# Kernel optimization log

Measured on AMD Instinct MI355X. Metric: run time of the kernel, lower is better.

Reference implementation:

```python
import jax, jax.numpy as jnp
import numpy as np

N = 50000      # nodes
E = 1600000    # edges (avg degree 32)
G = 128        # graphs in batch
NE = 5         # spectral supports (edge_attr channels)
NIN = 16       # input node features
H = 64         # nout1 hidden width
NCLS = 6
BN_EPS = 1e-5


def setup_inputs() -> dict:
    key = jax.random.key(0)
    ks = jax.random.split(key, 12)
    s = 0.1  # weight init scale
    x = jax.random.normal(ks[0], (N, NIN), dtype=jnp.float32)
    edge_index = jax.random.randint(ks[1], (2, E), 0, N, dtype=jnp.int32)
    edge_attr = jax.random.normal(ks[2], (E, NE), dtype=jnp.float32)
    # sorted segment ids covering all G graphs (non-empty segments)
    batch = ((jnp.arange(N, dtype=jnp.int32) * G) // N).astype(jnp.int32)
    W1 = jax.random.normal(ks[3], (NE, NIN, H), dtype=jnp.float32) * s
    W2 = jax.random.normal(ks[4], (NE, H, H), dtype=jnp.float32) * s
    W3 = jax.random.normal(ks[5], (NE, H, H), dtype=jnp.float32) * s
    W4 = jax.random.normal(ks[6], (NE, H, H), dtype=jnp.float32) * s
    b1 = jnp.zeros((H,), jnp.float32)
    b2 = jnp.zeros((H,), jnp.float32)
    b3 = jnp.zeros((H,), jnp.float32)
    b4 = jnp.zeros((H,), jnp.float32)
    bn_gamma = jnp.ones((2 * H,), jnp.float32)
    bn_beta = jnp.zeros((2 * H,), jnp.float32)
    bn_mean = jax.random.normal(ks[7], (2 * H,), dtype=jnp.float32)
    bn_var = jax.random.uniform(ks[8], (2 * H,), dtype=jnp.float32) + 0.5
    fc_w = jax.random.normal(ks[9], (2 * H, NCLS), dtype=jnp.float32) * s
    fc_b = jnp.zeros((NCLS,), jnp.float32)
    return {"x": x, "edge_index": edge_index, "edge_attr": edge_attr,
            "batch": batch, "W1": W1, "b1": b1, "W2": W2, "b2": b2,
            "W3": W3, "b3": b3, "W4": W4, "b4": b4,
            "bn_gamma": bn_gamma, "bn_beta": bn_beta,
            "bn_mean": bn_mean, "bn_var": bn_var,
            "fc_w": fc_w, "fc_b": fc_b}


def spect_conv(x, src, dst, edge_attr, W, b):
    # SpectConv(selfconn=False): out = sum_k scatter_add(edge_attr[:,k]*x[src] -> dst) @ W[k] + b
    xs = x[src]  # [E, F] gather
    n = x.shape[0]
    out = jnp.zeros((n, W.shape[2]), x.dtype)
    for k in range(W.shape[0]):  # K=5 spectral supports
        h = jax.ops.segment_sum(edge_attr[:, k:k + 1] * xs, dst, num_segments=n)
        out = out + h @ W[k]
    return out + b


def reference(x, edge_index, edge_attr, batch, W1, b1, W2, b2, W3, b3, W4, b4,
              bn_gamma, bn_beta, bn_mean, bn_var, fc_w, fc_b):
    src, dst = edge_index[0], edge_index[1]
    h = jax.nn.relu(spect_conv(x, src, dst, edge_attr, W1, b1))
    h = jax.nn.relu(spect_conv(h, src, dst, edge_attr, W2, b2))
    h = jax.nn.relu(spect_conv(h, src, dst, edge_attr, W3, b3))
    h = jax.nn.relu(spect_conv(h, src, dst, edge_attr, W4, b4))
    pooled = jnp.concatenate([
        jax.ops.segment_sum(h, batch, num_segments=G),
        jax.ops.segment_max(h, batch, num_segments=G)], axis=1)  # [G, 2H]
    bn = (pooled - bn_mean) * jax.lax.rsqrt(bn_var + BN_EPS) * bn_gamma + bn_beta
    return jax.nn.log_softmax(bn @ fc_w + fc_b, axis=1)
```

## Files before the change

### kernel.cpp

```cpp
#include <hip/hip_runtime.h>


#define Nn   50000
#define Ne   1600000
#define Gg   128
#define NEk  5
#define NINf 16
#define NCLSo 6
#define NB   196
#define NCPY 8

using short8 = __attribute__((ext_vector_type(8))) short;
using f32x4  = __attribute__((ext_vector_type(4))) float;

__device__ __forceinline__ float2 bf2u(unsigned u) {
    return make_float2(__uint_as_float(u << 16), __uint_as_float(u & 0xffff0000u));
}
__device__ __forceinline__ unsigned f2bf(float a, float b) {
    unsigned ua = __float_as_uint(a), ub = __float_as_uint(b);
    ua += 0x7fffu + ((ua >> 16) & 1u);
    ub += 0x7fffu + ((ub >> 16) & 1u);
    return (ua >> 16) | (ub & 0xffff0000u);
}
__device__ __forceinline__ unsigned short f2bf1(float a) {
    unsigned ua = __float_as_uint(a);
    ua += 0x7fffu + ((ua >> 16) & 1u);
    return (unsigned short)(ua >> 16);
}


__global__ void k_pad_x(const float* __restrict__ x, unsigned* __restrict__ h0) {
    int i = blockIdx.x * 256 + threadIdx.x;
    if (i >= Nn * 32) return;
    int n = i >> 5, p = i & 31;
    int f0 = 2 * p;
    float v0 = (f0 < NINf) ? x[n * NINf + f0] : 0.f;
    float v1 = (f0 + 1 < NINf) ? x[n * NINf + f0 + 1] : 0.f;
    h0[i] = f2bf(v0, v1);
}

__global__ void k_pad_w1(const float* __restrict__ W1, float* __restrict__ W1p) {
    int i = blockIdx.x * 256 + threadIdx.x;
    if (i >= NEk * 64 * 64) return;
    int h = i & 63, f = (i >> 6) & 63, k = i >> 12;
    W1p[i] = (f < NINf) ? W1[(k * NINf + f) * 64 + h] : 0.f;
}

__global__ void k_pack_b(const float* __restrict__ W, unsigned short* __restrict__ bhi,
                         unsigned short* __restrict__ blo) {
    int i = blockIdx.x * 256 + threadIdx.x;
    if (i >= 20480) return;
    int j = i & 7, lane = (i >> 3) & 63, t2 = i >> 9;
    int nt = t2 / 10, kstep = t2 - nt * 10;
    int k = kstep * 32 + (lane >> 4) * 8 + j;
    int col = nt * 16 + (lane & 15);
    float v = W[k * 64 + col];
    unsigned short hi = f2bf1(v);
    float fhi = __uint_as_float(((unsigned)hi) << 16);
    bhi[i] = hi;
    blo[i] = f2bf1(v - fhi);
}

__global__ void k_rank(const int* __restrict__ ei, int* __restrict__ deg8,
                       int* __restrict__ rank) {
    int e = blockIdx.x * 256 + threadIdx.x;
    if (e >= Ne) return;
    int c = blockIdx.x & (NCPY - 1);
    int r = atomicAdd(&deg8[c * Nn + ei[Ne + e]], 1);
    rank[e] = (c << 24) | r;
}

__global__ void k_sumdeg(int* __restrict__ deg8, int* __restrict__ deg) {
    int d = blockIdx.x * 256 + threadIdx.x;
    if (d >= Nn) return;
    int s = 0;
#pragma unroll
    for (int c = 0; c < NCPY; ++c) {
        int t = deg8[c * Nn + d];
        deg8[c * Nn + d] = s;
        s += t;
    }
    deg[d] = s;
}


__global__ void k_blocksum(const int* __restrict__ deg, int* __restrict__ bsum) {
    __shared__ int l[256];
    int t = threadIdx.x;
    int i = blockIdx.x * 256 + t;
    l[t] = (i < Nn) ? deg[i] : 0;
    __syncthreads();
    for (int off = 128; off > 0; off >>= 1) {
        if (t < off) l[t] += l[t + off];
        __syncthreads();
    }
    if (t == 0) bsum[blockIdx.x] = l[0];
}

__global__ void k_scanpart(const int* __restrict__ bsum, int* __restrict__ boff) {
    __shared__ int l[256];
    int t = threadIdx.x;
    int v = (t < NB) ? bsum[t] : 0;
    l[t] = v;
    __syncthreads();
    for (int off = 1; off < 256; off <<= 1) {
        int u = (t >= off) ? l[t - off] : 0;
        __syncthreads();
        l[t] += u;
        __syncthreads();
    }
    if (t < NB) boff[t] = l[t] - v;
}

__global__ void k_scanfinal(const int* __restrict__ deg, const int* __restrict__ boff,
                            int* __restrict__ rowstart) {
    __shared__ int l[256];
    int t = threadIdx.x;
    int i = blockIdx.x * 256 + t;
    int v = (i < Nn) ? deg[i] : 0;
    l[t] = v;
    __syncthreads();
    for (int off = 1; off < 256; off <<= 1) {
        int u = (t >= off) ? l[t - off] : 0;
        __syncthreads();
        l[t] += u;
        __syncthreads();
    }
    if (i <= Nn) rowstart[i] = boff[blockIdx.x] + l[t] - v;
}

__global__ void k_place(const int* __restrict__ ei, const float* __restrict__ eattr,
                        const int* __restrict__ rowstart, const int* __restrict__ rank,
                        const int* __restrict__ deg8, uint4* __restrict__ recs) {
    int e = blockIdx.x * 256 + threadIdx.x;
    if (e >= Ne) return;
    int d = ei[Ne + e];
    int rk = rank[e];
    int c = rk >> 24, r = rk & 0xffffff;
    int pos = rowstart[d] + deg8[c * Nn + d] + r;
    const float* a = eattr + (size_t)e * 5;
    uint4 rr;
    rr.x = (unsigned)ei[e];
    rr.y = f2bf(a[0], a[1]);
    rr.z = f2bf(a[2], a[3]);
    rr.w = f2bf(a[4], 0.f);
    recs[pos] = rr;
}

__global__ void k_bounds(const int* __restrict__ batch, int* __restrict__ sg,
                         int* __restrict__ eg) {
    int n = blockIdx.x * 256 + threadIdx.x;
    if (n >= Nn) return;
    int g = batch[n];
    if (n == 0) sg[g] = 0;
    else {
        int gp = batch[n - 1];
        if (gp != g) { sg[g] = n; eg[gp] = n; }
    }
    if (n == Nn - 1) eg[g] = Nn;
}


__global__ __launch_bounds__(256) void k_aggregate(
    const unsigned* __restrict__ hin, const int* __restrict__ rowstart,
    const uint4* __restrict__ recs, unsigned* __restrict__ agg) {
    int lane = threadIdx.x & 63;
    int l = lane & 31, half = lane >> 5;
    int node = __builtin_amdgcn_readfirstlane((int)(blockIdx.x * 4 + (threadIdx.x >> 6)));
    int beg = rowstart[node], end = rowstart[node + 1];
    float2 c0 = {0.f, 0.f}, c1 = c0, c2 = c0, c3 = c0, c4 = c0;
    int ee = beg;
#define EDGE(E) { \
    uint4 r = recs[(E)]; \
    unsigned hx = hin[(size_t)(int)r.x * 32 + l]; \
    float2 xv = bf2u(hx); \
    float2 A01 = bf2u(r.y), A23 = bf2u(r.z); \
    float a4v = __uint_as_float(r.w << 16); \
    c0.x = fmaf(A01.x, xv.x, c0.x); c0.y = fmaf(A01.x, xv.y, c0.y); \
    c1.x = fmaf(A01.y, xv.x, c1.x); c1.y = fmaf(A01.y, xv.y, c1.y); \
    c2.x = fmaf(A23.x, xv.x, c2.x); c2.y = fmaf(A23.x, xv.y, c2.y); \
    c3.x = fmaf(A23.y, xv.x, c3.x); c3.y = fmaf(A23.y, xv.y, c3.y); \
    c4.x = fmaf(a4v,  xv.x, c4.x); c4.y = fmaf(a4v,  xv.y, c4.y); }
    for (; ee + 8 <= end; ee += 8) {
        EDGE(ee + half) EDGE(ee + 2 + half) EDGE(ee + 4 + half) EDGE(ee + 6 + half)
    }
    for (; ee + 2 <= end; ee += 2) { EDGE(ee + half) }
    if (ee < end) { if (half == 0) { EDGE(ee) } }
#undef EDGE
    c0.x += __shfl(c0.x, lane ^ 32); c0.y += __shfl(c0.y, lane ^ 32);
    c1.x += __shfl(c1.x, lane ^ 32); c1.y += __shfl(c1.y, lane ^ 32);
    c2.x += __shfl(c2.x, lane ^ 32); c2.y += __shfl(c2.y, lane ^ 32);
    c3.x += __shfl(c3.x, lane ^ 32); c3.y += __shfl(c3.y, lane ^ 32);
    c4.x += __shfl(c4.x, lane ^ 32); c4.y += __shfl(c4.y, lane ^ 32);
    if (half == 0) {
        unsigned* o = agg + (size_t)node * 160 + l;
        o[0]   = f2bf(c0.x, c0.y);
        o[32]  = f2bf(c1.x, c1.y);
        o[64]  = f2bf(c2.x, c2.y);
        o[96]  = f2bf(c3.x, c3.y);
        o[128] = f2bf(c4.x, c4.y);
    }
}

#define SPAD 41
__global__ __launch_bounds__(256) void k_transform(
    const uint4* __restrict__ A, const unsigned short* __restrict__ bhi,
    const unsigned short* __restrict__ blo, const float* __restrict__ bias,
    unsigned* __restrict__ outh) {
    __shared__ uint4 smem[64 * SPAD];
    int t = threadIdx.x;
    int lane = t & 63, wave = t >> 6;
    int m = lane & 15, quad = lane >> 4;
    int blk = blockIdx.x;

#pragma unroll
    for (int it = 0; it < 10; ++it) {
        int v = t + it * 256;
        int row = v / 40, off = v - row * 40;
        int node = blk * 64 + row;
        if (node >= Nn) node = Nn - 1;
        smem[row * SPAD + off] = A[(size_t)node * 40 + off];
    }
    __syncthreads();

    f32x4 acc0 = {0.f, 0.f, 0.f, 0.f}, acc1 = acc0, acc2 = acc0, acc3 = acc0;
    const uint4* arow = smem + (wave * 16 + m) * SPAD + quad;
#pragma unroll 2
    for (int ks = 0; ks < 10; ++ks) {
        short8 a = *(const short8*)(arow + ks * 4);
        size_t bb = ((size_t)ks * 64 + lane) * 8;
        short8 h0 = *(const short8*)(bhi + bb);
        short8 l0 = *(const short8*)(blo + bb);
        acc0 = __builtin_amdgcn_mfma_f32_16x16x32_bf16(a, h0, acc0, 0, 0, 0);
        acc0 = __builtin_amdgcn_mfma_f32_16x16x32_bf16(a, l0, acc0, 0, 0, 0);
        short8 h1 = *(const short8*)(bhi + bb + 5120);
        short8 l1 = *(const short8*)(blo + bb + 5120);
        acc1 = __builtin_amdgcn_mfma_f32_16x16x32_bf16(a, h1, acc1, 0, 0, 0);
        acc1 = __builtin_amdgcn_mfma_f32_16x16x32_bf16(a, l1, acc1, 0, 0, 0);
        short8 h2 = *(const short8*)(bhi + bb + 10240);
        short8 l2 = *(const short8*)(blo + bb + 10240);
        acc2 = __builtin_amdgcn_mfma_f32_16x16x32_bf16(a, h2, acc2, 0, 0, 0);
        acc2 = __builtin_amdgcn_mfma_f32_16x16x32_bf16(a, l2, acc2, 0, 0, 0);
        short8 h3 = *(const short8*)(bhi + bb + 15360);
        short8 l3 = *(const short8*)(blo + bb + 15360);
        acc3 = __builtin_amdgcn_mfma_f32_16x16x32_bf16(a, h3, acc3, 0, 0, 0);
        acc3 = __builtin_amdgcn_mfma_f32_16x16x32_bf16(a, l3, acc3, 0, 0, 0);
    }
    __syncthreads();

    float* Cs = (float*)smem;
#pragma unroll
    for (int r = 0; r < 4; ++r) {
        int base = wave * 1152 + (quad * 4 + r) * 72 + m;
        Cs[base]      = acc0[r];
        Cs[base + 16] = acc1[r];
        Cs[base + 32] = acc2[r];
        Cs[base + 48] = acc3[r];
    }
    __syncthreads();

    int row = t >> 2, grp = t & 3;
    int node = blk * 64 + row;
    if (node < Nn) {
        const float* cr = Cs + (row >> 4) * 1152 + (row & 15) * 72;
        unsigned o[8];
#pragma unroll
        for (int j = 0; j < 8; ++j) {
            int pp = grp * 8 + j;
            float v0 = fmaxf(cr[2 * pp]     + bias[2 * pp],     0.f);
            float v1 = fmaxf(cr[2 * pp + 1] + bias[2 * pp + 1], 0.f);
            o[j] = f2bf(v0, v1);
        }
        uint4* dst = (uint4*)(outh + (size_t)node * 32 + grp * 8);
        dst[0] = make_uint4(o[0], o[1], o[2], o[3]);
        dst[1] = make_uint4(o[4], o[5], o[6], o[7]);
    }
}


__global__ __launch_bounds__(256) void k_pool(const unsigned* __restrict__ h,
                                              const int* __restrict__ sg,
                                              const int* __restrict__ eg,
                                              float* __restrict__ pooled) {
    __shared__ float2 ls[256], lm[256];
    int g = blockIdx.x, t = threadIdx.x;
    int p = t & 31, q = t >> 5;
    int s = sg[g], e = eg[g];
    float2 sum = {0.f, 0.f}, mx = {0.f, 0.f};
    for (int n = s + q; n < e; n += 8) {
        float2 v = bf2u(h[(size_t)n * 32 + p]);
        sum.x += v.x; sum.y += v.y;
        mx.x = fmaxf(mx.x, v.x); mx.y = fmaxf(mx.y, v.y);
    }
    ls[t] = sum; lm[t] = mx;
    __syncthreads();
    if (t < 32) {
        float2 ss = ls[t], mm = lm[t];
        for (int i = 1; i < 8; ++i) {
            float2 a = ls[t + i * 32], b = lm[t + i * 32];
            ss.x += a.x; ss.y += a.y;
            mm.x = fmaxf(mm.x, b.x); mm.y = fmaxf(mm.y, b.y);
        }
        pooled[g * 128 + 2 * t]          = ss.x;
        pooled[g * 128 + 2 * t + 1]      = ss.y;
        pooled[g * 128 + 64 + 2 * t]     = mm.x;
        pooled[g * 128 + 64 + 2 * t + 1] = mm.y;
    }
}

__global__ void k_head(const float* __restrict__ pooled, const float* __restrict__ gamma,
                       const float* __restrict__ beta, const float* __restrict__ mean,
                       const float* __restrict__ var, const float* __restrict__ fcw,
                       const float* __restrict__ fcb, float* __restrict__ out) {
    __shared__ float y[128];
    __shared__ float lg[8];
    int g = blockIdx.x, c = threadIdx.x;
    float p = pooled[g * 128 + c];
    y[c] = (p - mean[c]) * rsqrtf(var[c] + 1e-5f) * gamma[c] + beta[c];
    __syncthreads();
    if (c < NCLSo) {
        float l = fcb[c];
        for (int i = 0; i < 128; ++i) l += y[i] * fcw[i * NCLSo + c];
        lg[c] = l;
    }
    __syncthreads();
    if (c == 0) {
        float m = lg[0];
        for (int j = 1; j < NCLSo; ++j) m = fmaxf(m, lg[j]);
        float se = 0.f;
        for (int j = 0; j < NCLSo; ++j) se += expf(lg[j] - m);
        float lse = m + logf(se);
        for (int j = 0; j < NCLSo; ++j) out[g * NCLSo + j] = lg[j] - lse;
    }
}


static inline size_t rup(size_t x) { return (x + 255) & ~(size_t)255; }

extern "C" void kernel_launch(void* const* d_in, const int* in_sizes, int n_in,
                              void* d_out, int out_size, void* d_ws, size_t ws_size,
                              hipStream_t stream) {
    const float* x     = (const float*)d_in[0];
    const int*   ei    = (const int*)d_in[1];
    const float* eattr = (const float*)d_in[2];
    const int*   batch = (const int*)d_in[3];
    const float* W1    = (const float*)d_in[4];
    const float* b1    = (const float*)d_in[5];
    const float* W2    = (const float*)d_in[6];
    const float* b2    = (const float*)d_in[7];
    const float* W3    = (const float*)d_in[8];
    const float* b3    = (const float*)d_in[9];
    const float* W4    = (const float*)d_in[10];
    const float* b4    = (const float*)d_in[11];
    const float* gamma = (const float*)d_in[12];
    const float* beta  = (const float*)d_in[13];
    const float* mean  = (const float*)d_in[14];
    const float* var   = (const float*)d_in[15];
    const float* fcw   = (const float*)d_in[16];
    const float* fcb   = (const float*)d_in[17];
    float* out = (float*)d_out;

    char* p = (char*)d_ws;
    auto take = [&](size_t bytes) { char* r = p; p += rup(bytes); return r; };
    int*            deg      = (int*)take((size_t)(Nn + 1) * 4);
    int*            deg8     = (int*)take((size_t)NCPY * Nn * 4);
    int*            rowstart = (int*)take((size_t)(Nn + 1) * 4);
    int*            bsum     = (int*)take((size_t)NB * 4);
    int*            boff     = (int*)take((size_t)NB * 4);
    int*            rank     = (int*)take((size_t)Ne * 4);
    uint4*          recs     = (uint4*)take((size_t)Ne * 16);
    unsigned*       hA       = (unsigned*)take((size_t)Nn * 32 * 4);
    unsigned*       hB       = (unsigned*)take((size_t)Nn * 32 * 4);
    unsigned*       agg      = (unsigned*)take((size_t)Nn * 160 * 4);
    float*          W1p      = (float*)take((size_t)NEk * 64 * 64 * 4);
    unsigned short* bhiA     = (unsigned short*)take((size_t)4 * 20480 * 2);
    unsigned short* bloA     = (unsigned short*)take((size_t)4 * 20480 * 2);
    float*          pooled   = (float*)take((size_t)Gg * 128 * 4);
    int*            sg       = (int*)take((size_t)Gg * 4);
    int*            eg       = (int*)take((size_t)Gg * 4);

    hipMemsetAsync(deg8, 0, (size_t)NCPY * Nn * 4, stream);

    k_pad_x<<<(Nn * 32 + 255) / 256, 256, 0, stream>>>(x, hA);
    k_pad_w1<<<(NEk * 64 * 64 + 255) / 256, 256, 0, stream>>>(W1, W1p);
    k_pack_b<<<80, 256, 0, stream>>>(W1p, bhiA,             bloA);
    k_pack_b<<<80, 256, 0, stream>>>(W2,  bhiA + 20480,     bloA + 20480);
    k_pack_b<<<80, 256, 0, stream>>>(W3,  bhiA + 2 * 20480, bloA + 2 * 20480);
    k_pack_b<<<80, 256, 0, stream>>>(W4,  bhiA + 3 * 20480, bloA + 3 * 20480);
    k_rank<<<(Ne + 255) / 256, 256, 0, stream>>>(ei, deg8, rank);
    k_sumdeg<<<(Nn + 255) / 256, 256, 0, stream>>>(deg8, deg);
    k_blocksum<<<NB, 256, 0, stream>>>(deg, bsum);
    k_scanpart<<<1, 256, 0, stream>>>(bsum, boff);
    k_scanfinal<<<NB, 256, 0, stream>>>(deg, boff, rowstart);
    k_place<<<(Ne + 255) / 256, 256, 0, stream>>>(ei, eattr, rowstart, rank, deg8, recs);
    k_bounds<<<(Nn + 255) / 256, 256, 0, stream>>>(batch, sg, eg);

    const float* bs[4] = { b1, b2, b3, b4 };
    unsigned* cur = hA;
    unsigned* nxt = hB;
    for (int L = 0; L < 4; ++L) {
        k_aggregate<<<Nn / 4, 256, 0, stream>>>(cur, rowstart, recs, agg);
        k_transform<<<(Nn + 63) / 64, 256, 0, stream>>>(
            (const uint4*)agg, bhiA + (size_t)L * 20480, bloA + (size_t)L * 20480,
            bs[L], nxt);
        unsigned* tmp = cur; cur = nxt; nxt = tmp;
    }

    k_pool<<<Gg, 256, 0, stream>>>(cur, sg, eg, pooled);
    k_head<<<Gg, 128, 0, stream>>>(pooled, gamma, beta, mean, var, fcw, fcb, out);
}
```

Baseline: 511.0 us.

## Replace global-atomic edge ranking with per-block shared-memory histograms

Edge ranking for the CSR build no longer uses global atomics on 8 copies of the degree array. Instead, 128 blocks each histogram a contiguous chunk of edges into packed 16-bit shared-memory counters, processing nodes in two halves. A column scan over the per-block counts then produces per-block offsets and degrees. This removes global atomic contention and the memset, but adds a 12.8MB count matrix that the column scan must read and write, and it runs only 128 blocks with two passes over the edges.

```diff
diff --git a/kernel.cpp b/kernel.cpp
--- a/kernel.cpp
+++ b/kernel.cpp
@@ -8,7 +8,8 @@
 #define NINf 16
 #define NCLSo 6
 #define NB   196
-#define NCPY 8
+#define RBK  128
+#define CHK  (Ne / RBK)
 
 using short8 = __attribute__((ext_vector_type(8))) short;
 using f32x4  = __attribute__((ext_vector_type(4))) float;
@@ -61,23 +62,40 @@
     blo[i] = f2bf1(v - fhi);
 }
 
-__global__ void k_rank(const int* __restrict__ ei, int* __restrict__ deg8,
-                       int* __restrict__ rank) {
-    int e = blockIdx.x * 256 + threadIdx.x;
-    if (e >= Ne) return;
-    int c = blockIdx.x & (NCPY - 1);
-    int r = atomicAdd(&deg8[c * Nn + ei[Ne + e]], 1);
-    rank[e] = (c << 24) | r;
-}
-
-__global__ void k_sumdeg(int* __restrict__ deg8, int* __restrict__ deg) {
+__global__ __launch_bounds__(1024) void k_rankhist(
+    const int* __restrict__ ei, unsigned short* __restrict__ lrank,
+    unsigned short* __restrict__ cnt ) {
+    __shared__ unsigned hist[12500];
+    int b = blockIdx.x, t = threadIdx.x;
+    int e0 = b * CHK;
+#pragma unroll 1
+    for (int h = 0; h < 2; ++h) {
+        int lo = h * 25000;
+        for (int w = t; w < 12500; w += 1024) hist[w] = 0;
+        __syncthreads();
+        for (int i = t; i < CHK; i += 1024) {
+            int d = ei[Ne + e0 + i];
+            unsigned dd = (unsigned)(d - lo);
+            if (dd < 25000u) {
+                unsigned old = atomicAdd(&hist[dd >> 1], (dd & 1u) ? 65536u : 1u);
+                lrank[e0 + i] = (unsigned short)(old >> (16 * (dd & 1u)));
+            }
+        }
+        __syncthreads();
+        unsigned* co = (unsigned*)(cnt + (size_t)b * Nn + lo);
+        for (int w = t; w < 12500; w += 1024) co[w] = hist[w];
+        __syncthreads();
+    }
+}
+
+__global__ void k_colscan(unsigned short* __restrict__ cnt, int* __restrict__ deg) {
     int d = blockIdx.x * 256 + threadIdx.x;
     if (d >= Nn) return;
     int s = 0;
-#pragma unroll
-    for (int c = 0; c < NCPY; ++c) {
-        int t = deg8[c * Nn + d];
-        deg8[c * Nn + d] = s;
+#pragma unroll 4
+    for (int b = 0; b < RBK; ++b) {
+        int t = cnt[(size_t)b * Nn + d];
+        cnt[(size_t)b * Nn + d] = (unsigned short)s;
         s += t;
     }
     deg[d] = s;
@@ -130,14 +148,15 @@
 }
 
 __global__ void k_place(const int* __restrict__ ei, const float* __restrict__ eattr,
-                        const int* __restrict__ rowstart, const int* __restrict__ rank,
-                        const int* __restrict__ deg8, uint4* __restrict__ recs) {
+                        const int* __restrict__ rowstart,
+                        const unsigned short* __restrict__ lrank,
+                        const unsigned short* __restrict__ cnt,
+                        uint4* __restrict__ recs) {
     int e = blockIdx.x * 256 + threadIdx.x;
     if (e >= Ne) return;
     int d = ei[Ne + e];
-    int rk = rank[e];
-    int c = rk >> 24, r = rk & 0xffffff;
-    int pos = rowstart[d] + deg8[c * Nn + d] + r;
+    int b = e / CHK;
+    int pos = rowstart[d] + cnt[(size_t)b * Nn + d] + lrank[e];
     const float* a = eattr + (size_t)e * 5;
     uint4 rr;
     rr.x = (unsigned)ei[e];
@@ -363,11 +382,11 @@
     char* p = (char*)d_ws;
     auto take = [&](size_t bytes) { char* r = p; p += rup(bytes); return r; };
     int*            deg      = (int*)take((size_t)(Nn + 1) * 4);
-    int*            deg8     = (int*)take((size_t)NCPY * Nn * 4);
+    unsigned short* cnt      = (unsigned short*)take((size_t)RBK * Nn * 2);
+    unsigned short* lrank    = (unsigned short*)take((size_t)Ne * 2);
     int*            rowstart = (int*)take((size_t)(Nn + 1) * 4);
     int*            bsum     = (int*)take((size_t)NB * 4);
     int*            boff     = (int*)take((size_t)NB * 4);
-    int*            rank     = (int*)take((size_t)Ne * 4);
     uint4*          recs     = (uint4*)take((size_t)Ne * 16);
     unsigned*       hA       = (unsigned*)take((size_t)Nn * 32 * 4);
     unsigned*       hB       = (unsigned*)take((size_t)Nn * 32 * 4);
@@ -379,20 +398,18 @@
     int*            sg       = (int*)take((size_t)Gg * 4);
     int*            eg       = (int*)take((size_t)Gg * 4);
 
-    hipMemsetAsync(deg8, 0, (size_t)NCPY * Nn * 4, stream);
-
+    k_rankhist<<<RBK, 1024, 0, stream>>>(ei, lrank, cnt);
     k_pad_x<<<(Nn * 32 + 255) / 256, 256, 0, stream>>>(x, hA);
     k_pad_w1<<<(NEk * 64 * 64 + 255) / 256, 256, 0, stream>>>(W1, W1p);
     k_pack_b<<<80, 256, 0, stream>>>(W1p, bhiA,             bloA);
     k_pack_b<<<80, 256, 0, stream>>>(W2,  bhiA + 20480,     bloA + 20480);
     k_pack_b<<<80, 256, 0, stream>>>(W3,  bhiA + 2 * 20480, bloA + 2 * 20480);
     k_pack_b<<<80, 256, 0, stream>>>(W4,  bhiA + 3 * 20480, bloA + 3 * 20480);
-    k_rank<<<(Ne + 255) / 256, 256, 0, stream>>>(ei, deg8, rank);
-    k_sumdeg<<<(Nn + 255) / 256, 256, 0, stream>>>(deg8, deg);
+    k_colscan<<<NB, 256, 0, stream>>>(cnt, deg);
     k_blocksum<<<NB, 256, 0, stream>>>(deg, bsum);
     k_scanpart<<<1, 256, 0, stream>>>(bsum, boff);
     k_scanfinal<<<NB, 256, 0, stream>>>(deg, boff, rowstart);
-    k_place<<<(Ne + 255) / 256, 256, 0, stream>>>(ei, eattr, rowstart, rank, deg8, recs);
+    k_place<<<(Ne + 255) / 256, 256, 0, stream>>>(ei, eattr, rowstart, lrank, cnt, recs);
     k_bounds<<<(Nn + 255) / 256, 256, 0, stream>>>(batch, sg, eg);
 
     const float* bs[4] = { b1, b2, b3, b4 };
```

Result: faster. 479.0 us (-6.3%).
